# Kernel tuning notes

Measured on AMD Instinct MI355X. Metric: run time of the kernel, lower is better.

The kernel has to match this reference:

```python
import jax, jax.numpy as jnp
import numpy as np

B, S, D, H = 2, 2048, 768, 12
HD = D // H


def setup_inputs() -> dict:
    key = jax.random.key(0)
    ks = jax.random.split(key, 11)
    scale = 1.0 / np.sqrt(D)
    return {
        "query": jax.random.normal(ks[0], (B, S, D), jnp.float32),
        "key_": jax.random.normal(ks[1], (B, S, D), jnp.float32),
        "value": jax.random.normal(ks[2], (B, S, D), jnp.float32),
        "Wq": jax.random.normal(ks[3], (D, D), jnp.float32) * scale,
        "bq": jnp.zeros((D,), jnp.float32),
        "Wk": jax.random.normal(ks[4], (D, D), jnp.float32) * scale,
        "bk": jnp.zeros((D,), jnp.float32),
        "Wv": jax.random.normal(ks[5], (D, D), jnp.float32) * scale,
        "bv": jnp.zeros((D,), jnp.float32),
        "Wo": jax.random.normal(ks[6], (D, D), jnp.float32) * scale,
        "bo": jnp.zeros((D,), jnp.float32),
    }


def reference(query, key_, value, Wq, bq, Wk, bk, Wv, bv, Wo, bo):
    # Linear projections (W stored as [in, out]); dropout = identity (eval)
    def split_heads(x):
        # [B, S, D] -> [B, H, S, HD]
        return x.reshape(B, S, H, HD).transpose(0, 2, 1, 3)

    Q = split_heads(query @ Wq + bq)
    K = split_heads(key_ @ Wk + bk)
    V = split_heads(value @ Wv + bv)

    inv_sqrt_dk = 1.0 / jnp.sqrt(jnp.asarray(HD, Q.dtype))
    score = jnp.einsum("bhqd,bhkd->bhqk", Q, K) * inv_sqrt_dk  # [B,H,S,S]
    prob = jax.nn.softmax(score, axis=-1)  # source bug: mask is never applied
    out = jnp.einsum("bhqk,bhkd->bhqd", prob, V)  # [B,H,S,HD]
    out = out.transpose(0, 2, 1, 3).reshape(B, S, D)
    return out @ Wo + bo
```

## Files before the change

kernel.cpp:

```cpp
#include <hip/hip_runtime.h>
#include <hip/hip_bf16.h>

#define BB 2
#define SS 2048
#define DDIM 768
#define NH 12
#define HD 64
#define MTOT (BB*SS)

constexpr float QSCALE = 0.125f * 1.44269504088896340736f;

typedef __bf16 bf16_t;
typedef __bf16 bf16x8 __attribute__((ext_vector_type(8)));
typedef __bf16 bf16x4 __attribute__((ext_vector_type(4)));
typedef float  f32x4  __attribute__((ext_vector_type(4)));

static __device__ __forceinline__ f32x4 mfma16(bf16x8 a, bf16x8 b, f32x4 c) {
    return __builtin_amdgcn_mfma_f32_16x16x32_bf16(a, b, c, 0, 0, 0);
}

typedef __attribute__((address_space(3))) unsigned int lds_u32;
typedef __attribute__((address_space(1))) const unsigned int glob_u32;
static __device__ __forceinline__ void gload16(const bf16_t* g, bf16_t* l) {
    __builtin_amdgcn_global_load_lds((glob_u32*)g, (lds_u32*)l, 16, 0, 0);
}

__global__ __launch_bounds__(256) void prep_all(
    const float* __restrict__ Wq, const float* __restrict__ Wk,
    const float* __restrict__ Wv, const float* __restrict__ Wo,
    const float* __restrict__ q, const float* __restrict__ k_,
    bf16_t* __restrict__ Wt, bf16_t* __restrict__ Xb)
{
    const int z = blockIdx.z, tid = threadIdx.x;
    if (z < 4) {
        if (blockIdx.x >= 24 || blockIdx.y >= 24) return;
        __shared__ float tile[32][33];
        const float* W = (z == 0) ? Wq : (z == 1) ? Wk : (z == 2) ? Wv : Wo;
        int n0 = blockIdx.x * 32, k0 = blockIdx.y * 32;
        int tx = tid & 31, ty = tid >> 5;
#pragma unroll
        for (int i = 0; i < 4; i++) {
            int k = ty + i * 8;
            tile[k][tx] = W[(size_t)(k0 + k) * DDIM + n0 + tx];
        }
        __syncthreads();
        bf16_t* out = Wt + (size_t)z * DDIM * DDIM;
#pragma unroll
        for (int i = 0; i < 4; i++) {
            int n = ty + i * 8;
            out[(size_t)(n0 + n) * DDIM + k0 + tx] = (bf16_t)tile[tx][n];
        }
    } else {
        const float* src = (z == 4) ? q : k_;
        size_t base = ((size_t)(blockIdx.y * 48 + blockIdx.x)) * 2048 + (size_t)tid * 8;
        f32x4 v0 = *(const f32x4*)&src[base];
        f32x4 v1 = *(const f32x4*)&src[base + 4];
        bf16x8 o;
#pragma unroll
        for (int i = 0; i < 4; i++) { o[i] = (bf16_t)v0[i]; o[i + 4] = (bf16_t)v1[i]; }
        *(bf16x8*)&Xb[(size_t)(z - 4) * MTOT * DDIM + base] = o;
    }
}

__global__ __launch_bounds__(256) void gemm_qkv(
    const bf16_t* __restrict__ Xb, const float* __restrict__ vf,
    const float* __restrict__ bq, const float* __restrict__ bk, const float* __restrict__ bv,
    const bf16_t* __restrict__ Wt,
    bf16_t* __restrict__ Q, bf16_t* __restrict__ K, bf16_t* __restrict__ Vtg)
{
    __shared__ alignas(16) bf16_t As[128 * 32];
    __shared__ alignas(16) bf16_t Bs[128 * 32];
    const int z = blockIdx.z;
    const int m0 = blockIdx.y * 128, n0 = blockIdx.x * 128;
    const int tid = threadIdx.x, lane = tid & 63, w = tid >> 6;
    const int wm = (w >> 1) * 64, wn = (w & 1) * 64;
    const int quad = lane >> 4, l15 = lane & 15;

    const bf16_t* A  = Xb + (size_t)z * (MTOT * DDIM);
    const bf16_t* Bt = Wt + (size_t)z * (DDIM * DDIM);
    const int srow = w * 32 + (lane >> 2);
    const int sg   = ((lane & 3) ^ ((lane >> 3) & 3)) * 8;
    bf16_t* AsW = &As[w * 1024];
    bf16_t* BsW = &Bs[w * 1024];
    const int frow = tid >> 1, fhalf = tid & 1;

    f32x4 acc[4][4];
#pragma unroll
    for (int mt = 0; mt < 4; mt++)
#pragma unroll
        for (int nt = 0; nt < 4; nt++) { f32x4 zz = {0.f,0.f,0.f,0.f}; acc[mt][nt] = zz; }

    const int aslot = (quad ^ ((l15 >> 1) & 3)) * 8;

    for (int k0 = 0; k0 < DDIM; k0 += 32) {
        __syncthreads();
        if (z < 2) {
            const bf16_t* Ag = A + (size_t)(m0 + srow) * DDIM + k0 + sg;
            gload16(Ag, AsW);
            gload16(Ag + (size_t)16 * DDIM, AsW + 512);
        } else {
            const float* src = vf + (size_t)(m0 + frow) * DDIM + k0 + fhalf * 16;
            f32x4 v0 = *(const f32x4*)(src);
            f32x4 v1 = *(const f32x4*)(src + 4);
            f32x4 v2 = *(const f32x4*)(src + 8);
            f32x4 v3 = *(const f32x4*)(src + 12);
            bf16x8 o0, o1;
#pragma unroll
            for (int i = 0; i < 4; i++) {
                o0[i] = (bf16_t)v0[i]; o0[i + 4] = (bf16_t)v1[i];
                o1[i] = (bf16_t)v2[i]; o1[i + 4] = (bf16_t)v3[i];
            }
            int sw = (frow >> 1) & 3;
            *(bf16x8*)&As[frow * 32 + ((2 * fhalf)     ^ sw) * 8] = o0;
            *(bf16x8*)&As[frow * 32 + ((2 * fhalf + 1) ^ sw) * 8] = o1;
        }
        {
            const bf16_t* Bg = Bt + (size_t)(n0 + srow) * DDIM + k0 + sg;
            gload16(Bg, BsW);
            gload16(Bg + (size_t)16 * DDIM, BsW + 512);
        }
        __syncthreads();

        bf16x8 a[4], b[4];
#pragma unroll
        for (int mt = 0; mt < 4; mt++)
            a[mt] = *(const bf16x8*)&As[(wm + mt * 16 + l15) * 32 + aslot];
#pragma unroll
        for (int nt = 0; nt < 4; nt++)
            b[nt] = *(const bf16x8*)&Bs[(wn + nt * 16 + l15) * 32 + aslot];
#pragma unroll
        for (int mt = 0; mt < 4; mt++)
#pragma unroll
            for (int nt = 0; nt < 4; nt++)
                acc[mt][nt] = mfma16(a[mt], b[nt], acc[mt][nt]);
    }

    const float* bias = (z == 0) ? bq : (z == 1) ? bk : bv;
    float bvals[4];
#pragma unroll
    for (int nt = 0; nt < 4; nt++)
        bvals[nt] = bias[n0 + wn + nt * 16 + l15];

    if (z == 2) {
#pragma unroll
        for (int mt = 0; mt < 4; mt++) {
            int row0 = m0 + wm + mt * 16 + quad * 4;
#pragma unroll
            for (int nt = 0; nt < 4; nt++) {
                int col = n0 + wn + nt * 16 + l15;
                bf16x4 pk;
#pragma unroll
                for (int r = 0; r < 4; r++) pk[r] = (bf16_t)(acc[mt][nt][r] + bvals[nt]);
                *(bf16x4*)&Vtg[(size_t)col * MTOT + row0] = pk;
            }
        }
    } else {
        bf16_t* C = (z == 0) ? Q : K;
        float scale = (z == 0) ? QSCALE : 1.0f;
#pragma unroll
        for (int mt = 0; mt < 4; mt++) {
            int row0 = m0 + wm + mt * 16 + quad * 4;
#pragma unroll
            for (int nt = 0; nt < 4; nt++) {
                int col = n0 + wn + nt * 16 + l15;
#pragma unroll
                for (int r = 0; r < 4; r++)
                    C[(size_t)(row0 + r) * DDIM + col] = (bf16_t)((acc[mt][nt][r] + bvals[nt]) * scale);
            }
        }
    }
}

__global__ __launch_bounds__(256) void gemm_out(
    const bf16_t* __restrict__ Ab, const bf16_t* __restrict__ Bt,
    const float* __restrict__ bo, float* __restrict__ out)
{
    __shared__ alignas(16) bf16_t As[128 * 32];
    __shared__ alignas(16) bf16_t Bs[128 * 32];
    const int m0 = blockIdx.y * 128, n0 = blockIdx.x * 128;
    const int tid = threadIdx.x, lane = tid & 63, w = tid >> 6;
    const int wm = (w >> 1) * 64, wn = (w & 1) * 64;
    const int quad = lane >> 4, l15 = lane & 15;
    const int srow = w * 32 + (lane >> 2);
    const int sg   = ((lane & 3) ^ ((lane >> 3) & 3)) * 8;
    bf16_t* AsW = &As[w * 1024];
    bf16_t* BsW = &Bs[w * 1024];

    f32x4 acc[4][4];
#pragma unroll
    for (int mt = 0; mt < 4; mt++)
#pragma unroll
        for (int nt = 0; nt < 4; nt++) { f32x4 zz = {0.f,0.f,0.f,0.f}; acc[mt][nt] = zz; }

    const int aslot = (quad ^ ((l15 >> 1) & 3)) * 8;

    for (int k0 = 0; k0 < DDIM; k0 += 32) {
        __syncthreads();
        const bf16_t* Ag = Ab + (size_t)(m0 + srow) * DDIM + k0 + sg;
        gload16(Ag, AsW);
        gload16(Ag + (size_t)16 * DDIM, AsW + 512);
        const bf16_t* Bg = Bt + (size_t)(n0 + srow) * DDIM + k0 + sg;
        gload16(Bg, BsW);
        gload16(Bg + (size_t)16 * DDIM, BsW + 512);
        __syncthreads();

        bf16x8 a[4], b[4];
#pragma unroll
        for (int mt = 0; mt < 4; mt++)
            a[mt] = *(const bf16x8*)&As[(wm + mt * 16 + l15) * 32 + aslot];
#pragma unroll
        for (int nt = 0; nt < 4; nt++)
            b[nt] = *(const bf16x8*)&Bs[(wn + nt * 16 + l15) * 32 + aslot];
#pragma unroll
        for (int mt = 0; mt < 4; mt++)
#pragma unroll
            for (int nt = 0; nt < 4; nt++)
                acc[mt][nt] = mfma16(a[mt], b[nt], acc[mt][nt]);
    }

    float bvals[4];
#pragma unroll
    for (int nt = 0; nt < 4; nt++)
        bvals[nt] = bo[n0 + wn + nt * 16 + l15];
#pragma unroll
    for (int mt = 0; mt < 4; mt++) {
        int row0 = m0 + wm + mt * 16 + quad * 4;
#pragma unroll
        for (int nt = 0; nt < 4; nt++) {
            int col = n0 + wn + nt * 16 + l15;
#pragma unroll
            for (int r = 0; r < 4; r++)
                out[(size_t)(row0 + r) * DDIM + col] = acc[mt][nt][r] + bvals[nt];
        }
    }
}

__global__ __launch_bounds__(256) void attn_kernel(
    const bf16_t* __restrict__ Qb, const bf16_t* __restrict__ Kb,
    const bf16_t* __restrict__ Vtg, bf16_t* __restrict__ Ab)
{
    const int q0 = blockIdx.x * 64;
    const int h  = blockIdx.y;
    const int b  = blockIdx.z;
    const int tid = threadIdx.x, lane = tid & 63, w = tid >> 6;
    const int quad = lane >> 4, l15 = lane & 15;

    __shared__ union {
        struct {
            alignas(16) bf16_t Ks[128][72];
            alignas(16) bf16_t Vt[64][136];
            alignas(16) bf16_t Ps[64][136];
        } a;
        struct {
            alignas(16) float Obuf[2][64][68];
            float Lb[4][64];
        } m;
    } u;

    bf16x8 qf[4][2];
#pragma unroll
    for (int qt = 0; qt < 4; qt++) {
        const bf16_t* src = Qb + (size_t)(b * SS + q0 + qt * 16 + l15) * DDIM + h * HD;
#pragma unroll
        for (int kh = 0; kh < 2; kh++)
            qf[qt][kh] = *(const bf16x8*)(src + kh * 32 + quad * 8);
    }

    f32x4 o[4][4];
#pragma unroll
    for (int dt = 0; dt < 4; dt++)
#pragma unroll
        for (int qt = 0; qt < 4; qt++) { f32x4 z = {0.f,0.f,0.f,0.f}; o[dt][qt] = z; }
    float l_s[4];
#pragma unroll
    for (int qt = 0; qt < 4; qt++) l_s[qt] = 0.f;

    const int srow = tid >> 1, shalf = tid & 1;
    const int vrow = tid >> 2, vseg = tid & 3;
    const bf16_t* kbase = Kb + (size_t)(b * SS + srow) * DDIM + h * HD + shalf * 32;
    const bf16_t* vbase = Vtg + (size_t)(h * HD + vrow) * MTOT + b * SS + vseg * 32;

    for (int kt0 = 0; kt0 < SS; kt0 += 128) {
        __syncthreads();
        {
            const bf16_t* src = kbase + (size_t)kt0 * DDIM;
            bf16x8 k0v = *(const bf16x8*)(src);
            bf16x8 k1v = *(const bf16x8*)(src + 8);
            bf16x8 k2v = *(const bf16x8*)(src + 16);
            bf16x8 k3v = *(const bf16x8*)(src + 24);
            *(bf16x8*)&u.a.Ks[srow][shalf * 32]      = k0v;
            *(bf16x8*)&u.a.Ks[srow][shalf * 32 + 8]  = k1v;
            *(bf16x8*)&u.a.Ks[srow][shalf * 32 + 16] = k2v;
            *(bf16x8*)&u.a.Ks[srow][shalf * 32 + 24] = k3v;
        }
        {
            const bf16_t* src = vbase + kt0;
            bf16x8 v0v = *(const bf16x8*)(src);
            bf16x8 v1v = *(const bf16x8*)(src + 8);
            bf16x8 v2v = *(const bf16x8*)(src + 16);
            bf16x8 v3v = *(const bf16x8*)(src + 24);
            *(bf16x8*)&u.a.Vt[vrow][vseg * 32]      = v0v;
            *(bf16x8*)&u.a.Vt[vrow][vseg * 32 + 8]  = v1v;
            *(bf16x8*)&u.a.Vt[vrow][vseg * 32 + 16] = v2v;
            *(bf16x8*)&u.a.Vt[vrow][vseg * 32 + 24] = v3v;
        }
        __syncthreads();

        f32x4 s_[2][4];
#pragma unroll
        for (int kt = 0; kt < 2; kt++) {
            bf16x8 ak0 = *(const bf16x8*)&u.a.Ks[w * 32 + kt * 16 + l15][quad * 8];
            bf16x8 ak1 = *(const bf16x8*)&u.a.Ks[w * 32 + kt * 16 + l15][32 + quad * 8];
#pragma unroll
            for (int qt = 0; qt < 4; qt++) {
                f32x4 z = {0.f,0.f,0.f,0.f};
                z = mfma16(ak0, qf[qt][0], z);
                z = mfma16(ak1, qf[qt][1], z);
                s_[kt][qt] = z;
            }
        }

#pragma unroll
        for (int qt = 0; qt < 4; qt++) {
            float rs = l_s[qt];
#pragma unroll
            for (int kt = 0; kt < 2; kt++) {
                bf16x4 pk;
#pragma unroll
                for (int r = 0; r < 4; r++) {
                    float p = __builtin_amdgcn_exp2f(s_[kt][qt][r]);
                    rs += p;
                    pk[r] = (bf16_t)p;
                }
                *(bf16x4*)&u.a.Ps[qt * 16 + l15][w * 32 + kt * 16 + quad * 4] = pk;
            }
            l_s[qt] = rs;
        }

        bf16x8 av[4], bp[4];
#pragma unroll
        for (int dt = 0; dt < 4; dt++)
            av[dt] = *(const bf16x8*)&u.a.Vt[dt * 16 + l15][w * 32 + quad * 8];
#pragma unroll
        for (int qt = 0; qt < 4; qt++)
            bp[qt] = *(const bf16x8*)&u.a.Ps[qt * 16 + l15][w * 32 + quad * 8];
#pragma unroll
        for (int dt = 0; dt < 4; dt++)
#pragma unroll
            for (int qt = 0; qt < 4; qt++)
                o[dt][qt] = mfma16(av[dt], bp[qt], o[dt][qt]);
    }

#pragma unroll
    for (int qt = 0; qt < 4; qt++) {
        float rs = l_s[qt];
        rs += __shfl_xor(rs, 16, 64);
        rs += __shfl_xor(rs, 32, 64);
        l_s[qt] = rs;
    }
    __syncthreads();
    if (quad == 0) {
#pragma unroll
        for (int qt = 0; qt < 4; qt++)
            u.m.Lb[w][qt * 16 + l15] = l_s[qt];
    }
    __syncthreads();
    float lstar[4];
#pragma unroll
    for (int qt = 0; qt < 4; qt++) {
        int q = qt * 16 + l15;
        lstar[qt] = u.m.Lb[0][q] + u.m.Lb[1][q] + u.m.Lb[2][q] + u.m.Lb[3][q];
    }
    if (w >= 2) {
        float* dst = &u.m.Obuf[w - 2][lane][0];
#pragma unroll
        for (int dt = 0; dt < 4; dt++)
#pragma unroll
            for (int qt = 0; qt < 4; qt++)
                *(f32x4*)(dst + (dt * 4 + qt) * 4) = o[dt][qt];
    }
    __syncthreads();
    if (w < 2) {
        const float* src = &u.m.Obuf[w][lane][0];
#pragma unroll
        for (int dt = 0; dt < 4; dt++)
#pragma unroll
            for (int qt = 0; qt < 4; qt++)
                o[dt][qt] += *(const f32x4*)(src + (dt * 4 + qt) * 4);
    }
    __syncthreads();
    if (w == 1) {
        float* dst = &u.m.Obuf[0][lane][0];
#pragma unroll
        for (int dt = 0; dt < 4; dt++)
#pragma unroll
            for (int qt = 0; qt < 4; qt++)
                *(f32x4*)(dst + (dt * 4 + qt) * 4) = o[dt][qt];
    }
    __syncthreads();
    if (w == 0) {
        const float* src = &u.m.Obuf[0][lane][0];
#pragma unroll
        for (int dt = 0; dt < 4; dt++)
#pragma unroll
            for (int qt = 0; qt < 4; qt++)
                o[dt][qt] += *(const f32x4*)(src + (dt * 4 + qt) * 4);
#pragma unroll
        for (int qt = 0; qt < 4; qt++) {
            float inv = 1.f / lstar[qt];
            size_t rbase = (size_t)(b * SS + q0 + qt * 16 + l15) * DDIM + h * HD;
#pragma unroll
            for (int dt = 0; dt < 4; dt++) {
                bf16x4 pk;
#pragma unroll
                for (int r = 0; r < 4; r++) pk[r] = (bf16_t)(o[dt][qt][r] * inv);
                *(bf16x4*)&Ab[rbase + dt * 16 + quad * 4] = pk;
            }
        }
    }
}

extern "C" void kernel_launch(void* const* d_in, const int* in_sizes, int n_in,
                              void* d_out, int out_size, void* d_ws, size_t ws_size,
                              hipStream_t stream)
{
    const float* q  = (const float*)d_in[0];
    const float* k  = (const float*)d_in[1];
    const float* v  = (const float*)d_in[2];
    const float* Wq = (const float*)d_in[3];
    const float* bq = (const float*)d_in[4];
    const float* Wk = (const float*)d_in[5];
    const float* bk = (const float*)d_in[6];
    const float* Wv = (const float*)d_in[7];
    const float* bv = (const float*)d_in[8];
    const float* Wo = (const float*)d_in[9];
    const float* bo = (const float*)d_in[10];
    float* out = (float*)d_out;

    bf16_t* Wt  = (bf16_t*)d_ws;
    bf16_t* Xb  = Wt + (size_t)4 * DDIM * DDIM;
    bf16_t* Qs  = Xb + (size_t)2 * MTOT * DDIM;
    bf16_t* Ks  = Qs + (size_t)MTOT * DDIM;
    bf16_t* Vtg = Ks + (size_t)MTOT * DDIM;
    bf16_t* Ab  = Xb;

    prep_all<<<dim3(48, 32, 6), 256, 0, stream>>>(Wq, Wk, Wv, Wo, q, k, Wt, Xb);
    gemm_qkv<<<dim3(6, 32, 3), 256, 0, stream>>>(Xb, v, bq, bk, bv, Wt, Qs, Ks, Vtg);
    attn_kernel<<<dim3(SS / 64, NH, BB), 256, 0, stream>>>(Qs, Ks, Vtg, Ab);
    gemm_out<<<dim3(6, 32), 256, 0, stream>>>(Ab, Wt + (size_t)3 * DDIM * DDIM, bo, out);
}
```

Before: 222.0 us.

## Load K and V fragments directly from global memory, drop LDS staging

The attention kernel now reads each warp's K and V MFMA fragments straight from global memory instead of cooperatively staging 128-key tiles of K and V^T into shared memory behind two barriers per iteration. Shared memory shrinks to the P buffer, which is padded to 144 columns. The grid is also flattened to 1D with head/batch as the fastest-varying index, so blocks sharing a query tile but working on different heads run together and K/V for a given head is reused through L2. This removes LDS traffic and barriers and raises occupancy, but relies on cache hits for K/V loads that each warp now issues itself. P is still written to and read from LDS with no barrier between waves, which is only safe if each wave touches only its own columns.

Result: faster. 213.6 us (-3.8%).

```diff
diff --git a/kernel.cpp b/kernel.cpp
--- a/kernel.cpp
+++ b/kernel.cpp
@@ -239,17 +239,16 @@
     const bf16_t* __restrict__ Qb, const bf16_t* __restrict__ Kb,
     const bf16_t* __restrict__ Vtg, bf16_t* __restrict__ Ab)
 {
-    const int q0 = blockIdx.x * 64;
-    const int h  = blockIdx.y;
-    const int b  = blockIdx.z;
+    const int id = blockIdx.x;
+    const int hb = id % 24, qi = id / 24;
+    const int h = hb % NH, b = hb / NH;
+    const int q0 = qi * 64;
     const int tid = threadIdx.x, lane = tid & 63, w = tid >> 6;
     const int quad = lane >> 4, l15 = lane & 15;
 
     __shared__ union {
         struct {
-            alignas(16) bf16_t Ks[128][72];
-            alignas(16) bf16_t Vt[64][136];
-            alignas(16) bf16_t Ps[64][136];
+            alignas(16) bf16_t Ps[64][144];
         } a;
         struct {
             alignas(16) float Obuf[2][64][68];
@@ -275,42 +274,16 @@
 #pragma unroll
     for (int qt = 0; qt < 4; qt++) l_s[qt] = 0.f;
 
-    const int srow = tid >> 1, shalf = tid & 1;
-    const int vrow = tid >> 2, vseg = tid & 3;
-    const bf16_t* kbase = Kb + (size_t)(b * SS + srow) * DDIM + h * HD + shalf * 32;
-    const bf16_t* vbase = Vtg + (size_t)(h * HD + vrow) * MTOT + b * SS + vseg * 32;
+    const bf16_t* kfrag = Kb + (size_t)(b * SS + w * 32 + l15) * DDIM + h * HD + quad * 8;
+    const bf16_t* vfrag = Vtg + (size_t)(h * HD + l15) * MTOT + b * SS + w * 32 + quad * 8;
 
     for (int kt0 = 0; kt0 < SS; kt0 += 128) {
-        __syncthreads();
-        {
-            const bf16_t* src = kbase + (size_t)kt0 * DDIM;
-            bf16x8 k0v = *(const bf16x8*)(src);
-            bf16x8 k1v = *(const bf16x8*)(src + 8);
-            bf16x8 k2v = *(const bf16x8*)(src + 16);
-            bf16x8 k3v = *(const bf16x8*)(src + 24);
-            *(bf16x8*)&u.a.Ks[srow][shalf * 32]      = k0v;
-            *(bf16x8*)&u.a.Ks[srow][shalf * 32 + 8]  = k1v;
-            *(bf16x8*)&u.a.Ks[srow][shalf * 32 + 16] = k2v;
-            *(bf16x8*)&u.a.Ks[srow][shalf * 32 + 24] = k3v;
-        }
-        {
-            const bf16_t* src = vbase + kt0;
-            bf16x8 v0v = *(const bf16x8*)(src);
-            bf16x8 v1v = *(const bf16x8*)(src + 8);
-            bf16x8 v2v = *(const bf16x8*)(src + 16);
-            bf16x8 v3v = *(const bf16x8*)(src + 24);
-            *(bf16x8*)&u.a.Vt[vrow][vseg * 32]      = v0v;
-            *(bf16x8*)&u.a.Vt[vrow][vseg * 32 + 8]  = v1v;
-            *(bf16x8*)&u.a.Vt[vrow][vseg * 32 + 16] = v2v;
-            *(bf16x8*)&u.a.Vt[vrow][vseg * 32 + 24] = v3v;
-        }
-        __syncthreads();
-
         f32x4 s_[2][4];
 #pragma unroll
         for (int kt = 0; kt < 2; kt++) {
-            bf16x8 ak0 = *(const bf16x8*)&u.a.Ks[w * 32 + kt * 16 + l15][quad * 8];
-            bf16x8 ak1 = *(const bf16x8*)&u.a.Ks[w * 32 + kt * 16 + l15][32 + quad * 8];
+            const bf16_t* kr = kfrag + (size_t)(kt0 + kt * 16) * DDIM;
+            bf16x8 ak0 = *(const bf16x8*)(kr);
+            bf16x8 ak1 = *(const bf16x8*)(kr + 32);
 #pragma unroll
             for (int qt = 0; qt < 4; qt++) {
                 f32x4 z = {0.f,0.f,0.f,0.f};
@@ -337,10 +310,10 @@
             l_s[qt] = rs;
         }
 
-        bf16x8 av[4], bp[4];
-#pragma unroll
-        for (int dt = 0; dt < 4; dt++)
-            av[dt] = *(const bf16x8*)&u.a.Vt[dt * 16 + l15][w * 32 + quad * 8];
+        bf16x8 av8[4], bp[4];
+#pragma unroll
+        for (int dt = 0; dt < 4; dt++)
+            av8[dt] = *(const bf16x8*)(vfrag + (size_t)(dt * 16) * MTOT + kt0);
 #pragma unroll
         for (int qt = 0; qt < 4; qt++)
             bp[qt] = *(const bf16x8*)&u.a.Ps[qt * 16 + l15][w * 32 + quad * 8];
@@ -348,7 +321,7 @@
         for (int dt = 0; dt < 4; dt++)
 #pragma unroll
             for (int qt = 0; qt < 4; qt++)
-                o[dt][qt] = mfma16(av[dt], bp[qt], o[dt][qt]);
+                o[dt][qt] = mfma16(av8[dt], bp[qt], o[dt][qt]);
     }
 
 #pragma unroll
@@ -446,6 +419,6 @@
 
     prep_all<<<dim3(48, 32, 6), 256, 0, stream>>>(Wq, Wk, Wv, Wo, q, k, Wt, Xb);
     gemm_qkv<<<dim3(6, 32, 3), 256, 0, stream>>>(Xb, v, bq, bk, bv, Wt, Qs, Ks, Vtg);
-    attn_kernel<<<dim3(SS / 64, NH, BB), 256, 0, stream>>>(Qs, Ks, Vtg, Ab);
+    attn_kernel<<<dim3((SS / 64) * NH * BB), 256, 0, stream>>>(Qs, Ks, Vtg, Ab);
     gemm_out<<<dim3(6, 32), 256, 0, stream>>>(Ab, Wt + (size_t)3 * DDIM * DDIM, bo, out);
 }
```
